# Kernel optimization log

Measured on AMD Instinct MI355X. Metric: run time of the kernel, lower is better.

Reference implementation:

```python
import jax, jax.numpy as jnp
import numpy as np

H, HID = 2, 64
N_USER, N_POST, N_ENT = 50000, 100000, 20000
EDGES = [("publish", 100000, N_USER, N_POST), ("repost", 200000, N_USER, N_POST), ("contain", 200000, N_POST, N_ENT), ("interact", 400000, N_USER, N_USER), ("follow", 400000, N_USER, N_USER), ("similar", 250000, N_POST, N_POST)]


def setup_inputs() -> dict:
    key = jax.random.key(0)
    ks = iter(jax.random.split(key, 64))
    d = {}
    d["x_post"] = jax.random.normal(next(ks), (N_POST, 768), jnp.float32)
    d["x_user"] = jax.random.normal(next(ks), (N_USER, 32), jnp.float32)
    d["x_entity"] = jax.random.normal(next(ks), (N_ENT, 64), jnp.float32)
    for name, E, ns, nd in EDGES:
        d["src_" + name] = jax.random.randint(next(ks), (E,), 0, ns, jnp.int32)
        d["dst_" + name] = jax.random.randint(next(ks), (E,), 0, nd, jnp.int32)
    def lin(k, o, i):
        return jax.random.normal(k, (o, i), jnp.float32) / np.sqrt(i)
    d["post_proj_w"] = lin(next(ks), HID, 768); d["post_proj_b"] = jnp.zeros((HID,), jnp.float32)
    d["user_proj_w"] = lin(next(ks), HID, 32); d["user_proj_b"] = jnp.zeros((HID,), jnp.float32)
    d["ent_proj_w"] = lin(next(ks), HID, 64); d["ent_proj_b"] = jnp.zeros((HID,), jnp.float32)
    # 2 layers x 6 relations of bipartite GATConv params, stacked
    d["W_src"] = jax.random.normal(next(ks), (2, 6, H * HID, HID), jnp.float32) / np.sqrt(HID)
    d["W_dst"] = jax.random.normal(next(ks), (2, 6, H * HID, HID), jnp.float32) / np.sqrt(HID)
    d["a_src"] = jax.random.normal(next(ks), (2, 6, H, HID), jnp.float32) * 0.1
    d["a_dst"] = jax.random.normal(next(ks), (2, 6, H, HID), jnp.float32) * 0.1
    d["gat_b"] = jnp.zeros((2, 6, HID), jnp.float32)
    d["cls_w1"] = lin(next(ks), HID // 2, HID); d["cls_b1"] = jnp.zeros((HID // 2,), jnp.float32)
    d["cls_w2"] = lin(next(ks), 1, HID // 2); d["cls_b2"] = jnp.zeros((1,), jnp.float32)
    return d


def _gat(x_src, x_dst, src, dst, w_s, w_d, a_s, a_d, b):
    """PyG GATConv, bipartite, heads=H, concat=False, no self loops."""
    n_dst = x_dst.shape[0]
    hs = (x_src @ w_s.T).reshape(-1, H, HID)   # [N_src, H, C]
    hd = (x_dst @ w_d.T).reshape(-1, H, HID)   # [N_dst, H, C]
    al_s = jnp.einsum("nhc,hc->nh", hs, a_s)
    al_d = jnp.einsum("nhc,hc->nh", hd, a_d)
    e = jax.nn.leaky_relu(al_s[src] + al_d[dst], negative_slope=0.2)  # [E, H]
    m = jax.ops.segment_max(e, dst, num_segments=n_dst)
    m = jnp.where(jnp.isfinite(m), m, 0.0)  # empty segments -> -inf, unused
    p = jnp.exp(e - m[dst])
    s = jax.ops.segment_sum(p, dst, num_segments=n_dst)
    alpha = p / (s[dst] + 1e-16)
    out = jax.ops.segment_sum(hs[src] * alpha[:, :, None], dst, num_segments=n_dst)
    return out.mean(axis=1) + b  # concat=False -> mean over heads, plus bias


def reference(x_post, x_user, x_entity, src_publish, dst_publish, src_repost, dst_repost, src_contain, dst_contain, src_interact, dst_interact, src_follow, dst_follow, src_similar, dst_similar, post_proj_w, post_proj_b, user_proj_w, user_proj_b, ent_proj_w, ent_proj_b, W_src, W_dst, a_src, a_dst, gat_b, cls_w1, cls_b1, cls_w2, cls_b2):
    h_post = x_post @ post_proj_w.T + post_proj_b
    h_user = x_user @ user_proj_w.T + user_proj_b
    h_ent = x_entity @ ent_proj_w.T + ent_proj_b
    for l in range(2):
        def g(r, xs, xd, s, dd):
            return _gat(xs, xd, s, dd, W_src[l, r], W_dst[l, r], a_src[l, r], a_dst[l, r], gat_b[l, r])
        new_post = (g(0, h_user, h_post, src_publish, dst_publish)
                    + g(1, h_user, h_post, src_repost, dst_repost)
                    + g(5, h_post, h_post, src_similar, dst_similar))
        new_ent = g(2, h_post, h_ent, src_contain, dst_contain)
        new_user = (g(3, h_user, h_user, src_interact, dst_interact)
                    + g(4, h_user, h_user, src_follow, dst_follow))
        h_post, h_user, h_ent = jax.nn.relu(new_post), jax.nn.relu(new_user), jax.nn.relu(new_ent)
    h = jax.nn.relu(h_post @ cls_w1.T + cls_b1)  # dropout is eval-mode identity
    return (h @ cls_w2.T + cls_b2).squeeze(-1)
```

## Files before the change

kernel.cpp:

```cpp
#include <hip/hip_runtime.h>

#define NPOST 100000
#define NUSER 50000
#define NENT  20000
#define NDTOT 420000
#define EACT  1350000
#define NSCANBLK 206
#define NT_AL 150000

typedef short short8 __attribute__((ext_vector_type(8)));
typedef float f32x4 __attribute__((ext_vector_type(4)));
typedef unsigned short ushort4v __attribute__((ext_vector_type(4)));

static __device__ __forceinline__ unsigned short f2bf(float x){
  union { float f; unsigned u; } v; v.f = x;
  unsigned r = v.u + 0x7FFF + ((v.u >> 16) & 1);
  return (unsigned short)(r >> 16);
}
static __device__ __forceinline__ float bf2f(unsigned short h){
  union { unsigned u; float f; } v; v.u = ((unsigned)h) << 16;
  return v.f;
}

struct EdgeMeta {
  const int* src[6];
  const int* dst[6];
  int E[6];
  int degoff[6];
};

struct PrepArgs {
  const float *Wp, *Wu, *We, *Wsrc, *Wdst, *asrc, *adst, *gatb;
  unsigned short *WpH, *WpL, *WuH, *WuL, *WeH, *WeL, *lbH, *lbL;
  float *weff_s, *weff_d, *bsum;
};

__global__ void k_prep(PrepArgs P){
  int idx = blockIdx.x * blockDim.x + threadIdx.x;
  if (idx < 49152){
    float x = P.Wp[idx];
    unsigned short h = f2bf(x);
    P.WpH[idx] = h; P.WpL[idx] = f2bf(x - bf2f(h));
  } else if (idx < 51200){
    int i = idx - 49152;
    float x = P.Wu[i];
    unsigned short h = f2bf(x);
    P.WuH[i] = h; P.WuL[i] = f2bf(x - bf2f(h));
  } else if (idx < 55296){
    int i = idx - 51200;
    float x = P.We[i];
    unsigned short h = f2bf(x);
    P.WeH[i] = h; P.WeL[i] = f2bf(x - bf2f(h));
  } else if (idx < 153600){
    int i = idx - 55296;
    const int off[6]  = {0, 24576, 40960, 49152, 73728, 90112};
    const int Ks[6]   = {384, 256, 128, 384, 256, 128};
    int seg = 5;
    #pragma unroll
    for (int s = 4; s >= 0; s--) if (i < off[s + 1]) seg = s;
    int l = seg / 3, type = seg % 3;
    int K = Ks[seg];
    int rem = i - off[seg];
    int n = rem / K, k = rem - n * K;
    int slot = k >> 7, head = (k >> 6) & 1, kk = k & 63;
    int rel;
    if (type == 0)      rel = (slot == 0) ? 0 : (slot == 1 ? 1 : 5);
    else if (type == 1) rel = (slot == 0) ? 3 : 4;
    else                rel = 2;
    int m = l * 6 + rel;
    float x = P.Wsrc[(size_t)m * 8192 + (head * 64 + n) * 64 + kk];
    unsigned short h = f2bf(x);
    P.lbH[i] = h; P.lbL[i] = f2bf(x - bf2f(h));
  } else if (idx < 156672){
    int i = idx - 153600;
    const float* W; const float* a; float* o; int j;
    if (i < 1536){ W = P.Wsrc; a = P.asrc; o = P.weff_s; j = i; }
    else         { W = P.Wdst; a = P.adst; o = P.weff_d; j = i - 1536; }
    int m = j >> 7;
    int rem = j & 127;
    int hh = rem >> 6, k = rem & 63;
    const float* Wm = W + (size_t)m * 8192;
    const float* am = a + (size_t)m * 128;
    float acc = 0.f;
    #pragma unroll 8
    for (int c = 0; c < 64; c++)
      acc += Wm[(hh * 64 + c) * 64 + k] * am[hh * 64 + c];
    o[j] = acc;
  } else if (idx < 157056){
    int i = idx - 156672;
    int c = i & 63;
    int lt = i >> 6;
    int l = lt / 3, t = lt % 3;
    float v;
    if (t == 0)      v = P.gatb[(l*6+0)*64+c] + P.gatb[(l*6+1)*64+c] + P.gatb[(l*6+5)*64+c];
    else if (t == 1) v = P.gatb[(l*6+3)*64+c] + P.gatb[(l*6+4)*64+c];
    else             v = P.gatb[(l*6+2)*64+c];
    P.bsum[lt * 64 + c] = v;
  }
}


__global__ void k_hist(EdgeMeta em, int* __restrict__ deg){
  const int map[5] = {0, 1, 3, 4, 5};
  int r = map[blockIdx.y];
  int e = blockIdx.x * blockDim.x + threadIdx.x;
  if (e >= em.E[r]) return;
  atomicAdd(&deg[em.degoff[r] + em.dst[r][e]], 1);
}

__global__ __launch_bounds__(256) void k_scanA(const int* __restrict__ deg,
                                               int* __restrict__ rowstart,
                                               int* __restrict__ blocksum){
  __shared__ int sums[256];
  int t = threadIdx.x;
  int base = blockIdx.x * 2048 + t * 8;
  int v[8]; int s = 0;
  #pragma unroll
  for (int i = 0; i < 8; i++){
    int j = base + i;
    v[i] = (j < NDTOT) ? deg[j] : 0;
    s += v[i];
  }
  sums[t] = s;
  __syncthreads();
  for (int off = 1; off < 256; off <<= 1){
    int x = (t >= off) ? sums[t - off] : 0;
    __syncthreads();
    sums[t] += x;
    __syncthreads();
  }
  int excl = (t > 0) ? sums[t - 1] : 0;
  if (t == 255) blocksum[blockIdx.x] = sums[255];
  int run = excl;
  #pragma unroll
  for (int i = 0; i < 8; i++){
    int j = base + i;
    if (j < NDTOT) rowstart[j] = run;
    run += v[i];
  }
}

__global__ __launch_bounds__(256) void k_scanB(int* __restrict__ blocksum){
  __shared__ int s[256];
  int t = threadIdx.x;
  s[t] = (t < NSCANBLK) ? blocksum[t] : 0;
  __syncthreads();
  for (int off = 1; off < 256; off <<= 1){
    int x = (t >= off) ? s[t - off] : 0;
    __syncthreads();
    s[t] += x;
    __syncthreads();
  }
  int excl = (t > 0) ? s[t - 1] : 0;
  if (t < NSCANBLK) blocksum[t] = excl;
}

__global__ void k_scanC(int* __restrict__ rowstart, const int* __restrict__ blocksum,
                        int* __restrict__ cursor){
  int j = blockIdx.x * blockDim.x + threadIdx.x;
  if (j < NDTOT){
    int v = rowstart[j] + blocksum[j >> 11];
    rowstart[j] = v;
    cursor[j] = v;
  }
  if (j == 0) rowstart[NDTOT] = EACT;
}

__global__ void k_scatter(EdgeMeta em, int* __restrict__ cursor,
                          int* __restrict__ csr_src, int* __restrict__ csr_row){
  const int map[5] = {0, 1, 3, 4, 5};
  int r = map[blockIdx.y];
  int e = blockIdx.x * blockDim.x + threadIdx.x;
  if (e >= em.E[r]) return;
  int d = em.dst[r][e];
  int w = em.degoff[r] + d;
  int pos = atomicAdd(&cursor[w], 1);
  csr_src[pos] = em.src[r][e];
  csr_row[pos] = w;
}


struct AlArgs {
  const float *h0, *h1;
  const float *ws, *wd;
  float *als, *ald;
  int layer;
};

static __device__ __forceinline__ float2 dot2w(const float4* hr, const float* __restrict__ w){
  const float4* w0 = (const float4*)w;
  const float4* w1 = (const float4*)(w + 64);
  float a0 = 0.f, a1 = 0.f;
  #pragma unroll
  for (int q = 0; q < 16; q++){
    float4 v = hr[q];
    float4 x0 = w0[q], x1 = w1[q];
    a0 += v.x*x0.x + v.y*x0.y + v.z*x0.z + v.w*x0.w;
    a1 += v.x*x1.x + v.y*x1.y + v.z*x1.z + v.w*x1.w;
  }
  return make_float2(a0, a1);
}

__global__ __launch_bounds__(256) void k_al_all(AlArgs A){
  int i = blockIdx.x * blockDim.x + threadIdx.x;
  if (i >= NT_AL) return;
  float4 hr[16];
  if (i < NPOST){
    int n = i;
    const float4* hp = (const float4*)(A.h0 + (size_t)n * 64);
    #pragma unroll
    for (int q = 0; q < 16; q++) hr[q] = hp[q];
    *(float2*)(A.als + (size_t)(300000 + n) * 2) = dot2w(hr, A.ws + 5 * 128);
    *(float2*)(A.ald + (size_t)(0      + n) * 2) = dot2w(hr, A.wd + 0 * 128);
    *(float2*)(A.ald + (size_t)(100000 + n) * 2) = dot2w(hr, A.wd + 1 * 128);
    *(float2*)(A.ald + (size_t)(320000 + n) * 2) = dot2w(hr, A.wd + 5 * 128);
  } else {
    int n = i - NPOST;
    const float4* hp = (const float4*)(A.h1 + (size_t)n * 64);
    #pragma unroll
    for (int q = 0; q < 16; q++) hr[q] = hp[q];
    *(float2*)(A.als + (size_t)(0      + n) * 2) = dot2w(hr, A.ws + 0 * 128);
    *(float2*)(A.als + (size_t)(50000  + n) * 2) = dot2w(hr, A.ws + 1 * 128);
    if (A.layer == 0){
      *(float2*)(A.als + (size_t)(200000 + n) * 2) = dot2w(hr, A.ws + 3 * 128);
      *(float2*)(A.als + (size_t)(250000 + n) * 2) = dot2w(hr, A.ws + 4 * 128);
      *(float2*)(A.ald + (size_t)(220000 + n) * 2) = dot2w(hr, A.wd + 3 * 128);
      *(float2*)(A.ald + (size_t)(270000 + n) * 2) = dot2w(hr, A.wd + 4 * 128);
    }
  }
}


struct EdgepArgs {
  const int *csr_src, *csr_row;
  const float *als, *ald;
  float2 *pcsr;
  int thr, off, nE;
};

__global__ __launch_bounds__(256) void k_edgep(EdgepArgs A){
  int e0 = blockIdx.x * blockDim.x + threadIdx.x;
  if (e0 >= A.nE) return;
  int e = e0 < A.thr ? e0 : e0 + A.off;
  int w = A.csr_row[e];
  int soffr;
  if      (w < 100000) soffr = 0;
  else if (w < 200000) soffr = 50000;
  else if (w < 270000) soffr = 200000;
  else if (w < 320000) soffr = 250000;
  else                 soffr = 300000;
  int sidx = A.csr_src[e];
  float2 as = *(const float2*)(A.als + (size_t)(soffr + sidx) * 2);
  float2 ad = *(const float2*)(A.ald + (size_t)w * 2);
  float e0v = as.x + ad.x, e1v = as.y + ad.y;
  e0v = e0v > 0.f ? e0v : 0.2f * e0v;
  e1v = e1v > 0.f ? e1v : 0.2f * e1v;
  A.pcsr[e] = make_float2(__expf(e0v), __expf(e1v));
}


static __device__ __forceinline__ int aswz(int row, int k){
  return row * 128 + ((((k >> 3) ^ (row & 7))) << 3) + (k & 7);
}

static __device__ __forceinline__ void agg_row(const int* __restrict__ csr_src,
                                               const float2* __restrict__ pcsr,
                                               const float* __restrict__ h, int l16,
                                               int rs, int re,
                                               f32x4& a0, f32x4& a1, float& s0, float& s1){
  int e = rs;
  for (; e + 3 < re; e += 4){
    int sa = csr_src[e];
    int sb = csr_src[e + 1];
    int sc = csr_src[e + 2];
    int sd = csr_src[e + 3];
    float2 pa = pcsr[e];
    float2 pb = pcsr[e + 1];
    float2 pc = pcsr[e + 2];
    float2 pd = pcsr[e + 3];
    f32x4 ha = *(const f32x4*)(h + (size_t)sa * 64 + l16 * 4);
    f32x4 hb = *(const f32x4*)(h + (size_t)sb * 64 + l16 * 4);
    f32x4 hc = *(const f32x4*)(h + (size_t)sc * 64 + l16 * 4);
    f32x4 hd = *(const f32x4*)(h + (size_t)sd * 64 + l16 * 4);
    #pragma unroll
    for (int j = 0; j < 4; j++){ a0[j] = fmaf(pa.x, ha[j], a0[j]); a1[j] = fmaf(pa.y, ha[j], a1[j]); }
    s0 += pa.x; s1 += pa.y;
    #pragma unroll
    for (int j = 0; j < 4; j++){ a0[j] = fmaf(pb.x, hb[j], a0[j]); a1[j] = fmaf(pb.y, hb[j], a1[j]); }
    s0 += pb.x; s1 += pb.y;
    #pragma unroll
    for (int j = 0; j < 4; j++){ a0[j] = fmaf(pc.x, hc[j], a0[j]); a1[j] = fmaf(pc.y, hc[j], a1[j]); }
    s0 += pc.x; s1 += pc.y;
    #pragma unroll
    for (int j = 0; j < 4; j++){ a0[j] = fmaf(pd.x, hd[j], a0[j]); a1[j] = fmaf(pd.y, hd[j], a1[j]); }
    s0 += pd.x; s1 += pd.y;
  }
  for (; e + 1 < re; e += 2){
    int sa = csr_src[e];
    int sb = csr_src[e + 1];
    float2 pa = pcsr[e];
    float2 pb = pcsr[e + 1];
    f32x4 ha = *(const f32x4*)(h + (size_t)sa * 64 + l16 * 4);
    f32x4 hb = *(const f32x4*)(h + (size_t)sb * 64 + l16 * 4);
    #pragma unroll
    for (int j = 0; j < 4; j++){ a0[j] = fmaf(pa.x, ha[j], a0[j]); a1[j] = fmaf(pa.y, ha[j], a1[j]); }
    s0 += pa.x; s1 += pa.y;
    #pragma unroll
    for (int j = 0; j < 4; j++){ a0[j] = fmaf(pb.x, hb[j], a0[j]); a1[j] = fmaf(pb.y, hb[j], a1[j]); }
    s0 += pb.x; s1 += pb.y;
  }
  if (e < re){
    int sa = csr_src[e];
    float2 pa = pcsr[e];
    f32x4 ha = *(const f32x4*)(h + (size_t)sa * 64 + l16 * 4);
    #pragma unroll
    for (int j = 0; j < 4; j++){ a0[j] = fmaf(pa.x, ha[j], a0[j]); a1[j] = fmaf(pa.y, ha[j], a1[j]); }
    s0 += pa.x; s1 += pa.y;
  }
}

struct FJob {
  const unsigned short *BH, *BL;
  const float *bias;
  float *C;
  int N, nslots, K;
  int wb0, wb1, wb2;
  int ss0, ss1, ss2;
};
struct FArgs {
  const int *rowstart, *csr_src;
  const float2 *pcsr;
  const float *h0, *h1;
  FJob j0, j1;
  int nb0;
};

__global__ __launch_bounds__(256) void k_fused(FArgs A){
  __shared__ __align__(16) unsigned short sAh[64 * 128];
  __shared__ __align__(16) unsigned short sAl[64 * 128];
  int b = blockIdx.x;
  FJob J = (b < A.nb0) ? A.j0 : A.j1;
  int boff = (b < A.nb0) ? 0 : A.nb0;
  int r0 = (b - boff) * 64;
  int t = threadIdx.x;
  int w = t >> 6, lane = t & 63;
  int q = lane >> 4, m15 = lane & 15;
  int g2 = t >> 4, l16 = t & 15;
  int wr = w & 1, wc = w >> 1;
  f32x4 acc[2][2];
  #pragma unroll
  for (int i = 0; i < 2; i++)
    #pragma unroll
    for (int j = 0; j < 2; j++)
      acc[i][j] = (f32x4){0.f, 0.f, 0.f, 0.f};

  for (int s = 0; s < J.nslots; s++){
    int wbase = (s == 0) ? J.wb0 : ((s == 1) ? J.wb1 : J.wb2);
    int ssel  = (s == 0) ? J.ss0 : ((s == 1) ? J.ss1 : J.ss2);
    const float* h = ssel ? A.h1 : A.h0;
    for (int rr = g2; rr < 64; rr += 16){
      int grow = r0 + rr;
      int rs = 0, re = 0;
      if (grow < J.N){
        int wg = wbase + grow;
        rs = A.rowstart[wg];
        re = A.rowstart[wg + 1];
      }
      f32x4 a0 = (f32x4){0.f,0.f,0.f,0.f};
      f32x4 a1 = (f32x4){0.f,0.f,0.f,0.f};
      float s0 = 0.f, s1 = 0.f;
      agg_row(A.csr_src, A.pcsr, h, l16, rs, re, a0, a1, s0, s1);
      float r0v = s0 > 0.f ? 0.5f / s0 : 0.f;
      float r1v = s1 > 0.f ? 0.5f / s1 : 0.f;
      ushort4v H0, H1, L0, L1;
      #pragma unroll
      for (int j = 0; j < 4; j++){
        float v0 = a0[j] * r0v;
        float v1 = a1[j] * r1v;
        unsigned short h0v = f2bf(v0); H0[j] = h0v; L0[j] = f2bf(v0 - bf2f(h0v));
        unsigned short h1v = f2bf(v1); H1[j] = h1v; L1[j] = f2bf(v1 - bf2f(h1v));
      }
      *(ushort4v*)(sAh + aswz(rr, l16 * 4))      = H0;
      *(ushort4v*)(sAh + aswz(rr, 64 + l16 * 4)) = H1;
      *(ushort4v*)(sAl + aswz(rr, l16 * 4))      = L0;
      *(ushort4v*)(sAl + aswz(rr, 64 + l16 * 4)) = L1;
    }
    __syncthreads();
    #pragma unroll
    for (int kc = 0; kc < 4; kc++){
      int gk = s * 128 + kc * 32;
      short8 ah[2], al_[2];
      #pragma unroll
      for (int i = 0; i < 2; i++){
        int mrow = wr * 32 + i * 16 + m15;
        ah[i]  = *(const short8*)(sAh + aswz(mrow, kc * 32 + q * 8));
        al_[i] = *(const short8*)(sAl + aswz(mrow, kc * 32 + q * 8));
      }
      #pragma unroll
      for (int j = 0; j < 2; j++){
        int bn = wc * 32 + j * 16 + m15;
        short8 bh = *(const short8*)(J.BH + (size_t)bn * J.K + gk + q * 8);
        short8 bl = *(const short8*)(J.BL + (size_t)bn * J.K + gk + q * 8);
        #pragma unroll
        for (int i = 0; i < 2; i++){
          acc[i][j] = __builtin_amdgcn_mfma_f32_16x16x32_bf16(ah[i],  bh, acc[i][j], 0, 0, 0);
          acc[i][j] = __builtin_amdgcn_mfma_f32_16x16x32_bf16(ah[i],  bl, acc[i][j], 0, 0, 0);
          acc[i][j] = __builtin_amdgcn_mfma_f32_16x16x32_bf16(al_[i], bh, acc[i][j], 0, 0, 0);
        }
      }
    }
    __syncthreads();
  }
  #pragma unroll
  for (int j = 0; j < 2; j++){
    int col = wc * 32 + j * 16 + m15;
    float bv = J.bias[col];
    #pragma unroll
    for (int i = 0; i < 2; i++){
      #pragma unroll
      for (int r = 0; r < 4; r++){
        int row = r0 + wr * 32 + i * 16 + q * 4 + r;
        if (row < J.N){
          float vv = acc[i][j][r] + bv;
          J.C[(size_t)row * 64 + col] = vv > 0.f ? vv : 0.f;
        }
      }
    }
  }
}


static __device__ __forceinline__ int swz(int row, int k){
  return row * 32 + ((((k >> 3) ^ ((row >> 2) & 3))) << 3) + (k & 7);
}

struct GemmJob {
  const float* A32;
  const unsigned short* AH; const unsigned short* AL;
  const unsigned short* BH; const unsigned short* BL;
  const float* bias; float* C;
  int N; int K;
};
struct GemmJobs { GemmJob j0, j1, j2; int nb0, nb1; };

template<int ASRC, int RELU>
__global__ __launch_bounds__(256) void k_mfgemm3(GemmJobs G){
  __shared__ __align__(16) unsigned short sAh[128 * 32];
  __shared__ __align__(16) unsigned short sAl[128 * 32];
  __shared__ __align__(16) unsigned short sBh[64 * 32];
  __shared__ __align__(16) unsigned short sBl[64 * 32];
  int b = blockIdx.x;
  GemmJob jb = G.j0;
  int boff = 0;
  if (b >= G.nb1){ jb = G.j2; boff = G.nb1; }
  else if (b >= G.nb0){ jb = G.j1; boff = G.nb0; }
  const float* A32 = jb.A32;
  const unsigned short* AH = jb.AH;
  const unsigned short* AL = jb.AL;
  const unsigned short* BH = jb.BH;
  const unsigned short* BL = jb.BL;
  int N = jb.N, K = jb.K;

  int t = threadIdx.x;
  int w = t >> 6, lane = t & 63;
  int q = lane >> 4, m15 = lane & 15;
  int r0 = (b - boff) * 128;
  f32x4 acc[2][4];
  #pragma unroll
  for (int i = 0; i < 2; i++)
    #pragma unroll
    for (int j = 0; j < 4; j++)
      acc[i][j] = (f32x4){0.f, 0.f, 0.f, 0.f};

  int arow = t >> 1, akb = (t & 1) * 16;
  int brow = t >> 2, bkb = (t & 3) * 8;

  for (int k0 = 0; k0 < K; k0 += 32){
    int gr = r0 + arow;
    if (ASRC == 0){
      float v[16];
      if (gr < N){
        const float4* ap = (const float4*)(A32 + (size_t)gr * K + k0 + akb);
        #pragma unroll
        for (int i = 0; i < 4; i++){
          float4 f = ap[i];
          v[i*4+0] = f.x; v[i*4+1] = f.y; v[i*4+2] = f.z; v[i*4+3] = f.w;
        }
      } else {
        #pragma unroll
        for (int i = 0; i < 16; i++) v[i] = 0.f;
      }
      short8 h0, h1, l0, l1;
      #pragma unroll
      for (int i = 0; i < 8; i++){
        unsigned short hh = f2bf(v[i]);
        h0[i] = (short)hh; l0[i] = (short)f2bf(v[i] - bf2f(hh));
        unsigned short hj = f2bf(v[8+i]);
        h1[i] = (short)hj; l1[i] = (short)f2bf(v[8+i] - bf2f(hj));
      }
      *(short8*)(sAh + swz(arow, akb))     = h0;
      *(short8*)(sAh + swz(arow, akb + 8)) = h1;
      *(short8*)(sAl + swz(arow, akb))     = l0;
      *(short8*)(sAl + swz(arow, akb + 8)) = l1;
    } else {
      short8 h0 = {0,0,0,0,0,0,0,0}, h1 = {0,0,0,0,0,0,0,0};
      short8 l0 = {0,0,0,0,0,0,0,0}, l1 = {0,0,0,0,0,0,0,0};
      if (gr < N){
        const short8* hp = (const short8*)(AH + (size_t)gr * K + k0 + akb);
        const short8* lp = (const short8*)(AL + (size_t)gr * K + k0 + akb);
        h0 = hp[0]; h1 = hp[1];
        l0 = lp[0]; l1 = lp[1];
      }
      *(short8*)(sAh + swz(arow, akb))     = h0;
      *(short8*)(sAh + swz(arow, akb + 8)) = h1;
      *(short8*)(sAl + swz(arow, akb))     = l0;
      *(short8*)(sAl + swz(arow, akb + 8)) = l1;
    }
    {
      short8 bh = *(const short8*)(BH + (size_t)brow * K + k0 + bkb);
      short8 bl = *(const short8*)(BL + (size_t)brow * K + k0 + bkb);
      *(short8*)(sBh + swz(brow, bkb)) = bh;
      *(short8*)(sBl + swz(brow, bkb)) = bl;
    }
    __syncthreads();
    short8 ah[2], al_[2];
    #pragma unroll
    for (int i = 0; i < 2; i++){
      int mrow = w * 32 + i * 16 + m15;
      ah[i]  = *(const short8*)(sAh + swz(mrow, q * 8));
      al_[i] = *(const short8*)(sAl + swz(mrow, q * 8));
    }
    #pragma unroll
    for (int j = 0; j < 4; j++){
      int bn = j * 16 + m15;
      short8 bh = *(const short8*)(sBh + swz(bn, q * 8));
      short8 bl = *(const short8*)(sBl + swz(bn, q * 8));
      #pragma unroll
      for (int i = 0; i < 2; i++){
        acc[i][j] = __builtin_amdgcn_mfma_f32_16x16x32_bf16(ah[i],  bh, acc[i][j], 0, 0, 0);
        acc[i][j] = __builtin_amdgcn_mfma_f32_16x16x32_bf16(ah[i],  bl, acc[i][j], 0, 0, 0);
        acc[i][j] = __builtin_amdgcn_mfma_f32_16x16x32_bf16(al_[i], bh, acc[i][j], 0, 0, 0);
      }
    }
    __syncthreads();
  }
  const float* bias = jb.bias;
  float* C = jb.C;
  #pragma unroll
  for (int j = 0; j < 4; j++){
    int col = j * 16 + m15;
    float bv = bias[col];
    #pragma unroll
    for (int i = 0; i < 2; i++){
      #pragma unroll
      for (int r = 0; r < 4; r++){
        int row = r0 + w * 32 + i * 16 + q * 4 + r;
        if (row < N){
          float vv = acc[i][j][r] + bv;
          if (RELU) vv = vv > 0.f ? vv : 0.f;
          C[(size_t)row * 64 + col] = vv;
        }
      }
    }
  }
}


__global__ __launch_bounds__(256) void k_classifier(const float* __restrict__ hpost,
                                                    const float* __restrict__ w1,
                                                    const float* __restrict__ b1,
                                                    const float* __restrict__ w2,
                                                    const float* __restrict__ b2,
                                                    float* __restrict__ out, int N){
  __shared__ float w1s[32 * 64];
  __shared__ float b1s[32];
  __shared__ float w2s[32];
  for (int i = threadIdx.x; i < 2048; i += 256) w1s[i] = w1[i];
  if (threadIdx.x < 32){
    b1s[threadIdx.x] = b1[threadIdx.x];
    w2s[threadIdx.x] = w2[threadIdx.x];
  }
  __syncthreads();
  float bias2 = b2[0];
  for (int n = blockIdx.x * blockDim.x + threadIdx.x; n < N; n += gridDim.x * blockDim.x){
    float4 hr[16];
    const float4* hp = (const float4*)(hpost + (size_t)n * 64);
    #pragma unroll
    for (int q = 0; q < 16; q++) hr[q] = hp[q];
    float o = bias2;
    #pragma unroll 4
    for (int j = 0; j < 32; j++){
      float dacc = b1s[j];
      const float4* wr = (const float4*)(w1s + j * 64);
      #pragma unroll
      for (int q = 0; q < 16; q++){
        float4 w = wr[q]; float4 v = hr[q];
        dacc += w.x*v.x + w.y*v.y + w.z*v.z + w.w*v.w;
      }
      dacc = dacc > 0.f ? dacc : 0.f;
      o += w2s[j] * dacc;
    }
    out[n] = o;
  }
}


static inline size_t align256(size_t x){ return (x + 255) & ~(size_t)255; }

extern "C" void kernel_launch(void* const* d_in, const int* in_sizes, int n_in,
                              void* d_out, int out_size, void* d_ws, size_t ws_size,
                              hipStream_t stream){
  (void)in_sizes; (void)n_in; (void)out_size; (void)ws_size;
  const float* x_post = (const float*)d_in[0];
  const float* x_user = (const float*)d_in[1];
  EdgeMeta em;
  for (int r = 0; r < 6; r++){
    em.src[r] = (const int*)d_in[3 + 2*r];
    em.dst[r] = (const int*)d_in[4 + 2*r];
  }
  const int Earr[6] = {100000, 200000, 200000, 400000, 400000, 250000};
  const int dgo[6]  = {0, 100000, 200000, 220000, 270000, 320000};
  for (int r = 0; r < 6; r++){ em.E[r] = Earr[r]; em.degoff[r] = dgo[r]; }

  const float* Wp   = (const float*)d_in[15]; const float* bp = (const float*)d_in[16];
  const float* Wu   = (const float*)d_in[17]; const float* bu = (const float*)d_in[18];
  const float* We   = (const float*)d_in[19];
  const float* Wsrc = (const float*)d_in[21];
  const float* Wdst = (const float*)d_in[22];
  const float* asrc = (const float*)d_in[23];
  const float* adst = (const float*)d_in[24];
  const float* gatb = (const float*)d_in[25];
  const float* cw1  = (const float*)d_in[26]; const float* cb1 = (const float*)d_in[27];
  const float* cw2  = (const float*)d_in[28]; const float* cb2 = (const float*)d_in[29];
  float* out = (float*)d_out;

  const int NN[2] = {NPOST, NUSER};

  char* p = (char*)d_ws;
  auto alloc = [&](size_t bytes){ char* r = p; p += align256(bytes); return r; };
  float* hA[2]; float* hB[2];
  for (int i = 0; i < 2; i++) hA[i] = (float*)alloc((size_t)NN[i] * 64 * 4);
  for (int i = 0; i < 2; i++) hB[i] = (float*)alloc((size_t)NN[i] * 64 * 4);
  float* als = (float*)alloc((size_t)400000 * 2 * 4);
  float* ald = (float*)alloc((size_t)NDTOT * 2 * 4);
  float* weff_s = (float*)alloc(1536 * 4);
  float* weff_d = (float*)alloc(1536 * 4);
  unsigned short* WpH = (unsigned short*)alloc(768 * 64 * 2);
  unsigned short* WpL = (unsigned short*)alloc(768 * 64 * 2);
  unsigned short* WuH = (unsigned short*)alloc(32 * 64 * 2);
  unsigned short* WuL = (unsigned short*)alloc(32 * 64 * 2);
  unsigned short* WeH = (unsigned short*)alloc(64 * 64 * 2);
  unsigned short* WeL = (unsigned short*)alloc(64 * 64 * 2);
  unsigned short* lbH = (unsigned short*)alloc(98304 * 2);
  unsigned short* lbL = (unsigned short*)alloc(98304 * 2);
  float* bsum   = (float*)alloc(6 * 64 * 4);
  int* deg      = (int*)alloc((size_t)NDTOT * 4);
  int* rowstart = (int*)alloc((size_t)(NDTOT + 1) * 4);
  int* cursor   = (int*)alloc((size_t)NDTOT * 4);
  int* csr_src  = (int*)alloc((size_t)EACT * 4);
  int* csr_row  = (int*)alloc((size_t)EACT * 4);
  float2* pcsr  = (float2*)alloc((size_t)EACT * 8);
  int* blocksum = (int*)alloc((size_t)NSCANBLK * 4);

  hipMemsetAsync(deg, 0, (size_t)NDTOT * 4, stream);
  k_hist<<<dim3(1563, 5), 256, 0, stream>>>(em, deg);
  k_scanA<<<NSCANBLK, 256, 0, stream>>>(deg, rowstart, blocksum);
  k_scanB<<<1, 256, 0, stream>>>(blocksum);
  k_scanC<<<(NDTOT + 255) / 256, 256, 0, stream>>>(rowstart, blocksum, cursor);
  k_scatter<<<dim3(1563, 5), 256, 0, stream>>>(em, cursor, csr_src, csr_row);

  PrepArgs P = {Wp, Wu, We, Wsrc, Wdst, asrc, adst, gatb,
                WpH, WpL, WuH, WuL, WeH, WeL, lbH, lbL,
                weff_s, weff_d, bsum};
  k_prep<<<614, 256, 0, stream>>>(P);

  GemmJobs GP;
  GP.j0 = {x_post, nullptr, nullptr, WpH, WpL, bp, hA[0], NPOST, 768};
  GP.j1 = {x_user, nullptr, nullptr, WuH, WuL, bu, hA[1], NUSER, 32};
  GP.j2 = GP.j1;
  GP.nb0 = 782; GP.nb1 = 1173;
  k_mfgemm3<0, 0><<<1173, 256, 0, stream>>>(GP);

  const int segoff[6] = {0, 24576, 40960, 49152, 73728, 90112};

  float* cur[2] = {hA[0], hA[1]};
  float* nxt[2] = {hB[0], hB[1]};

  for (int l = 0; l < 2; l++){
    AlArgs AA = {cur[0], cur[1], weff_s + l * 768, weff_d + l * 768, als, ald, l};
    k_al_all<<<(NT_AL + 255) / 256, 256, 0, stream>>>(AA);

    int nE  = (l == 0) ? EACT : 550000;
    int thr = (l == 0) ? EACT : 300000;
    int off = (l == 0) ? 0 : 800000;
    EdgepArgs EP = {csr_src, csr_row, als, ald, pcsr, thr, off, nE};
    k_edgep<<<(nE + 255) / 256, 256, 0, stream>>>(EP);

    FArgs FA;
    FA.rowstart = rowstart; FA.csr_src = csr_src; FA.pcsr = pcsr;
    FA.h0 = cur[0]; FA.h1 = cur[1];
    FA.j0 = {lbH + segoff[l*3+0], lbL + segoff[l*3+0], bsum + (l*3+0) * 64, nxt[0],
             NPOST, 3, 384, 0, 100000, 320000, 1, 1, 0};
    int grid;
    if (l == 0){
      FA.j1 = {lbH + segoff[l*3+1], lbL + segoff[l*3+1], bsum + (l*3+1) * 64, nxt[1],
               NUSER, 2, 256, 220000, 270000, 0, 1, 1, 0};
      FA.nb0 = 1563; grid = 1563 + 782;
    } else {
      FA.j1 = FA.j0;
      FA.nb0 = 1563; grid = 1563;
    }
    k_fused<<<grid, 256, 0, stream>>>(FA);

    for (int i = 0; i < 2; i++){ float* tmp = cur[i]; cur[i] = nxt[i]; nxt[i] = tmp; }
  }

  k_classifier<<<(NPOST + 255) / 256, 256, 0, stream>>>(cur[0], cw1, cb1, cw2, cb2, out, NPOST);
}
```

Before: 583.0 us.

## Fuse edge-softmax logits into aggregation and classifier into last fused layer

```diff
diff --git a/kernel.cpp b/kernel.cpp
--- a/kernel.cpp
+++ b/kernel.cpp
@@ -166,8 +166,7 @@
   if (j == 0) rowstart[NDTOT] = EACT;
 }
 
-__global__ void k_scatter(EdgeMeta em, int* __restrict__ cursor,
-                          int* __restrict__ csr_src, int* __restrict__ csr_row){
+__global__ void k_scatter(EdgeMeta em, int* __restrict__ cursor, int* __restrict__ csr_src){
   const int map[5] = {0, 1, 3, 4, 5};
   int r = map[blockIdx.y];
   int e = blockIdx.x * blockDim.x + threadIdx.x;
@@ -176,7 +175,6 @@
   int w = em.degoff[r] + d;
   int pos = atomicAdd(&cursor[w], 1);
   csr_src[pos] = em.src[r][e];
-  csr_row[pos] = w;
 }
 
 
@@ -231,91 +229,71 @@
 }
 
 
-struct EdgepArgs {
-  const int *csr_src, *csr_row;
-  const float *als, *ald;
-  float2 *pcsr;
-  int thr, off, nE;
-};
-
-__global__ __launch_bounds__(256) void k_edgep(EdgepArgs A){
-  int e0 = blockIdx.x * blockDim.x + threadIdx.x;
-  if (e0 >= A.nE) return;
-  int e = e0 < A.thr ? e0 : e0 + A.off;
-  int w = A.csr_row[e];
-  int soffr;
-  if      (w < 100000) soffr = 0;
-  else if (w < 200000) soffr = 50000;
-  else if (w < 270000) soffr = 200000;
-  else if (w < 320000) soffr = 250000;
-  else                 soffr = 300000;
-  int sidx = A.csr_src[e];
-  float2 as = *(const float2*)(A.als + (size_t)(soffr + sidx) * 2);
-  float2 ad = *(const float2*)(A.ald + (size_t)w * 2);
-  float e0v = as.x + ad.x, e1v = as.y + ad.y;
-  e0v = e0v > 0.f ? e0v : 0.2f * e0v;
-  e1v = e1v > 0.f ? e1v : 0.2f * e1v;
-  A.pcsr[e] = make_float2(__expf(e0v), __expf(e1v));
-}
-
-
 static __device__ __forceinline__ int aswz(int row, int k){
   return row * 128 + ((((k >> 3) ^ (row & 7))) << 3) + (k & 7);
 }
 
+static __device__ __forceinline__ void edge_p(const int* __restrict__ csr_src,
+                                              const float* __restrict__ als, float2 ad,
+                                              int e, int& s_out, float& px, float& py){
+  int sidx = csr_src[e];
+  float2 as = *(const float2*)(als + (size_t)sidx * 2);
+  float e0 = as.x + ad.x, e1 = as.y + ad.y;
+  e0 = e0 > 0.f ? e0 : 0.2f * e0;
+  e1 = e1 > 0.f ? e1 : 0.2f * e1;
+  px = __expf(e0); py = __expf(e1);
+  s_out = sidx;
+}
+
 static __device__ __forceinline__ void agg_row(const int* __restrict__ csr_src,
-                                               const float2* __restrict__ pcsr,
+                                               const float* __restrict__ als, float2 ad,
                                                const float* __restrict__ h, int l16,
                                                int rs, int re,
                                                f32x4& a0, f32x4& a1, float& s0, float& s1){
   int e = rs;
   for (; e + 3 < re; e += 4){
-    int sa = csr_src[e];
-    int sb = csr_src[e + 1];
-    int sc = csr_src[e + 2];
-    int sd = csr_src[e + 3];
-    float2 pa = pcsr[e];
-    float2 pb = pcsr[e + 1];
-    float2 pc = pcsr[e + 2];
-    float2 pd = pcsr[e + 3];
+    int sa, sb, sc, sd; float pax, pay, pbx, pby, pcx, pcy, pdx, pdy;
+    edge_p(csr_src, als, ad, e,     sa, pax, pay);
+    edge_p(csr_src, als, ad, e + 1, sb, pbx, pby);
+    edge_p(csr_src, als, ad, e + 2, sc, pcx, pcy);
+    edge_p(csr_src, als, ad, e + 3, sd, pdx, pdy);
     f32x4 ha = *(const f32x4*)(h + (size_t)sa * 64 + l16 * 4);
     f32x4 hb = *(const f32x4*)(h + (size_t)sb * 64 + l16 * 4);
     f32x4 hc = *(const f32x4*)(h + (size_t)sc * 64 + l16 * 4);
     f32x4 hd = *(const f32x4*)(h + (size_t)sd * 64 + l16 * 4);
     #pragma unroll
-    for (int j = 0; j < 4; j++){ a0[j] = fmaf(pa.x, ha[j], a0[j]); a1[j] = fmaf(pa.y, ha[j], a1[j]); }
-    s0 += pa.x; s1 += pa.y;
-    #pragma unroll
-    for (int j = 0; j < 4; j++){ a0[j] = fmaf(pb.x, hb[j], a0[j]); a1[j] = fmaf(pb.y, hb[j], a1[j]); }
-    s0 += pb.x; s1 += pb.y;
-    #pragma unroll
-    for (int j = 0; j < 4; j++){ a0[j] = fmaf(pc.x, hc[j], a0[j]); a1[j] = fmaf(pc.y, hc[j], a1[j]); }
-    s0 += pc.x; s1 += pc.y;
-    #pragma unroll
-    for (int j = 0; j < 4; j++){ a0[j] = fmaf(pd.x, hd[j], a0[j]); a1[j] = fmaf(pd.y, hd[j], a1[j]); }
-    s0 += pd.x; s1 += pd.y;
+    for (int j = 0; j < 4; j++){ a0[j] = fmaf(pax, ha[j], a0[j]); a1[j] = fmaf(pay, ha[j], a1[j]); }
+    s0 += pax; s1 += pay;
+    #pragma unroll
+    for (int j = 0; j < 4; j++){ a0[j] = fmaf(pbx, hb[j], a0[j]); a1[j] = fmaf(pby, hb[j], a1[j]); }
+    s0 += pbx; s1 += pby;
+    #pragma unroll
+    for (int j = 0; j < 4; j++){ a0[j] = fmaf(pcx, hc[j], a0[j]); a1[j] = fmaf(pcy, hc[j], a1[j]); }
+    s0 += pcx; s1 += pcy;
+    #pragma unroll
+    for (int j = 0; j < 4; j++){ a0[j] = fmaf(pdx, hd[j], a0[j]); a1[j] = fmaf(pdy, hd[j], a1[j]); }
+    s0 += pdx; s1 += pdy;
   }
   for (; e + 1 < re; e += 2){
-    int sa = csr_src[e];
-    int sb = csr_src[e + 1];
-    float2 pa = pcsr[e];
-    float2 pb = pcsr[e + 1];
+    int sa, sb; float pax, pay, pbx, pby;
+    edge_p(csr_src, als, ad, e,     sa, pax, pay);
+    edge_p(csr_src, als, ad, e + 1, sb, pbx, pby);
     f32x4 ha = *(const f32x4*)(h + (size_t)sa * 64 + l16 * 4);
     f32x4 hb = *(const f32x4*)(h + (size_t)sb * 64 + l16 * 4);
     #pragma unroll
-    for (int j = 0; j < 4; j++){ a0[j] = fmaf(pa.x, ha[j], a0[j]); a1[j] = fmaf(pa.y, ha[j], a1[j]); }
-    s0 += pa.x; s1 += pa.y;
-    #pragma unroll
-    for (int j = 0; j < 4; j++){ a0[j] = fmaf(pb.x, hb[j], a0[j]); a1[j] = fmaf(pb.y, hb[j], a1[j]); }
-    s0 += pb.x; s1 += pb.y;
+    for (int j = 0; j < 4; j++){ a0[j] = fmaf(pax, ha[j], a0[j]); a1[j] = fmaf(pay, ha[j], a1[j]); }
+    s0 += pax; s1 += pay;
+    #pragma unroll
+    for (int j = 0; j < 4; j++){ a0[j] = fmaf(pbx, hb[j], a0[j]); a1[j] = fmaf(pby, hb[j], a1[j]); }
+    s0 += pbx; s1 += pby;
   }
   if (e < re){
-    int sa = csr_src[e];
-    float2 pa = pcsr[e];
+    int sa; float pax, pay;
+    edge_p(csr_src, als, ad, e, sa, pax, pay);
     f32x4 ha = *(const f32x4*)(h + (size_t)sa * 64 + l16 * 4);
     #pragma unroll
-    for (int j = 0; j < 4; j++){ a0[j] = fmaf(pa.x, ha[j], a0[j]); a1[j] = fmaf(pa.y, ha[j], a1[j]); }
-    s0 += pa.x; s1 += pa.y;
+    for (int j = 0; j < 4; j++){ a0[j] = fmaf(pax, ha[j], a0[j]); a1[j] = fmaf(pay, ha[j], a1[j]); }
+    s0 += pax; s1 += pay;
   }
 }
 
@@ -326,18 +304,23 @@
   int N, nslots, K;
   int wb0, wb1, wb2;
   int ss0, ss1, ss2;
+  int as0, as1, as2;
 };
 struct FArgs {
   const int *rowstart, *csr_src;
-  const float2 *pcsr;
+  const float *als, *ald;
   const float *h0, *h1;
   FJob j0, j1;
   int nb0;
+  const float *cw1, *cb1, *cw2, *cb2;
+  float *out;
 };
 
+template<int CLS>
 __global__ __launch_bounds__(256) void k_fused(FArgs A){
-  __shared__ __align__(16) unsigned short sAh[64 * 128];
-  __shared__ __align__(16) unsigned short sAl[64 * 128];
+  __shared__ __align__(16) unsigned short sbuf[2 * 64 * 128];
+  unsigned short* sAh = sbuf;
+  unsigned short* sAl = sbuf + 64 * 128;
   int b = blockIdx.x;
   FJob J = (b < A.nb0) ? A.j0 : A.j1;
   int boff = (b < A.nb0) ? 0 : A.nb0;
@@ -357,19 +340,23 @@
   for (int s = 0; s < J.nslots; s++){
     int wbase = (s == 0) ? J.wb0 : ((s == 1) ? J.wb1 : J.wb2);
     int ssel  = (s == 0) ? J.ss0 : ((s == 1) ? J.ss1 : J.ss2);
+    int aoff  = (s == 0) ? J.as0 : ((s == 1) ? J.as1 : J.as2);
     const float* h = ssel ? A.h1 : A.h0;
+    const float* als = A.als + (size_t)aoff * 2;
     for (int rr = g2; rr < 64; rr += 16){
       int grow = r0 + rr;
       int rs = 0, re = 0;
+      float2 ad = make_float2(0.f, 0.f);
       if (grow < J.N){
         int wg = wbase + grow;
         rs = A.rowstart[wg];
         re = A.rowstart[wg + 1];
+        ad = *(const float2*)(A.ald + (size_t)wg * 2);
       }
       f32x4 a0 = (f32x4){0.f,0.f,0.f,0.f};
       f32x4 a1 = (f32x4){0.f,0.f,0.f,0.f};
       float s0 = 0.f, s1 = 0.f;
-      agg_row(A.csr_src, A.pcsr, h, l16, rs, re, a0, a1, s0, s1);
+      agg_row(A.csr_src, als, ad, h, l16, rs, re, a0, a1, s0, s1);
       float r0v = s0 > 0.f ? 0.5f / s0 : 0.f;
       float r1v = s1 > 0.f ? 0.5f / s1 : 0.f;
       ushort4v H0, H1, L0, L1;
@@ -411,19 +398,66 @@
     }
     __syncthreads();
   }
-  #pragma unroll
-  for (int j = 0; j < 2; j++){
-    int col = wc * 32 + j * 16 + m15;
-    float bv = J.bias[col];
-    #pragma unroll
-    for (int i = 0; i < 2; i++){
+  if (!CLS){
+    #pragma unroll
+    for (int j = 0; j < 2; j++){
+      int col = wc * 32 + j * 16 + m15;
+      float bv = J.bias[col];
       #pragma unroll
-      for (int r = 0; r < 4; r++){
-        int row = r0 + wr * 32 + i * 16 + q * 4 + r;
-        if (row < J.N){
+      for (int i = 0; i < 2; i++){
+        #pragma unroll
+        for (int r = 0; r < 4; r++){
+          int row = r0 + wr * 32 + i * 16 + q * 4 + r;
+          if (row < J.N){
+            float vv = acc[i][j][r] + bv;
+            J.C[(size_t)row * 64 + col] = vv > 0.f ? vv : 0.f;
+          }
+        }
+      }
+    }
+  } else {
+    float* ht  = (float*)sbuf;
+    float* w1s = ht + 64 * 68;
+    float* b1s = w1s + 2048;
+    float* w2s = b1s + 32;
+    #pragma unroll
+    for (int j = 0; j < 2; j++){
+      int col = wc * 32 + j * 16 + m15;
+      float bv = J.bias[col];
+      #pragma unroll
+      for (int i = 0; i < 2; i++){
+        #pragma unroll
+        for (int r = 0; r < 4; r++){
+          int lrow = wr * 32 + i * 16 + q * 4 + r;
           float vv = acc[i][j][r] + bv;
-          J.C[(size_t)row * 64 + col] = vv > 0.f ? vv : 0.f;
+          ht[lrow * 68 + col] = vv > 0.f ? vv : 0.f;
         }
+      }
+    }
+    for (int i = t; i < 2048; i += 256) w1s[i] = A.cw1[i];
+    if (t < 32){ b1s[t] = A.cb1[t]; w2s[t] = A.cw2[t]; }
+    __syncthreads();
+    if (t < 64){
+      int row = r0 + t;
+      if (row < J.N){
+        float4 hr[16];
+        const float4* hp = (const float4*)(ht + t * 68);
+        #pragma unroll
+        for (int q16 = 0; q16 < 16; q16++) hr[q16] = hp[q16];
+        float o = A.cb2[0];
+        #pragma unroll 4
+        for (int j = 0; j < 32; j++){
+          float dacc = b1s[j];
+          const float4* wr_ = (const float4*)(w1s + j * 64);
+          #pragma unroll
+          for (int q16 = 0; q16 < 16; q16++){
+            float4 wv = wr_[q16]; float4 v = hr[q16];
+            dacc += wv.x*v.x + wv.y*v.y + wv.z*v.z + wv.w*v.w;
+          }
+          dacc = dacc > 0.f ? dacc : 0.f;
+          o += w2s[j] * dacc;
+        }
+        A.out[row] = o;
       }
     }
   }
@@ -562,45 +596,6 @@
         }
       }
     }
-  }
-}
-
-
-__global__ __launch_bounds__(256) void k_classifier(const float* __restrict__ hpost,
-                                                    const float* __restrict__ w1,
-                                                    const float* __restrict__ b1,
-                                                    const float* __restrict__ w2,
-                                                    const float* __restrict__ b2,
-                                                    float* __restrict__ out, int N){
-  __shared__ float w1s[32 * 64];
-  __shared__ float b1s[32];
-  __shared__ float w2s[32];
-  for (int i = threadIdx.x; i < 2048; i += 256) w1s[i] = w1[i];
-  if (threadIdx.x < 32){
-    b1s[threadIdx.x] = b1[threadIdx.x];
-    w2s[threadIdx.x] = w2[threadIdx.x];
-  }
-  __syncthreads();
-  float bias2 = b2[0];
-  for (int n = blockIdx.x * blockDim.x + threadIdx.x; n < N; n += gridDim.x * blockDim.x){
-    float4 hr[16];
-    const float4* hp = (const float4*)(hpost + (size_t)n * 64);
-    #pragma unroll
-    for (int q = 0; q < 16; q++) hr[q] = hp[q];
-    float o = bias2;
-    #pragma unroll 4
-    for (int j = 0; j < 32; j++){
-      float dacc = b1s[j];
-      const float4* wr = (const float4*)(w1s + j * 64);
-      #pragma unroll
-      for (int q = 0; q < 16; q++){
-        float4 w = wr[q]; float4 v = hr[q];
-        dacc += w.x*v.x + w.y*v.y + w.z*v.z + w.w*v.w;
-      }
-      dacc = dacc > 0.f ? dacc : 0.f;
-      o += w2s[j] * dacc;
-    }
-    out[n] = o;
   }
 }
 
@@ -658,8 +653,6 @@
   int* rowstart = (int*)alloc((size_t)(NDTOT + 1) * 4);
   int* cursor   = (int*)alloc((size_t)NDTOT * 4);
   int* csr_src  = (int*)alloc((size_t)EACT * 4);
-  int* csr_row  = (int*)alloc((size_t)EACT * 4);
-  float2* pcsr  = (float2*)alloc((size_t)EACT * 8);
   int* blocksum = (int*)alloc((size_t)NSCANBLK * 4);
 
   hipMemsetAsync(deg, 0, (size_t)NDTOT * 4, stream);
@@ -667,7 +660,7 @@
   k_scanA<<<NSCANBLK, 256, 0, stream>>>(deg, rowstart, blocksum);
   k_scanB<<<1, 256, 0, stream>>>(blocksum);
   k_scanC<<<(NDTOT + 255) / 256, 256, 0, stream>>>(rowstart, blocksum, cursor);
-  k_scatter<<<dim3(1563, 5), 256, 0, stream>>>(em, cursor, csr_src, csr_row);
+  k_scatter<<<dim3(1563, 5), 256, 0, stream>>>(em, cursor, csr_src);
 
   PrepArgs P = {Wp, Wu, We, Wsrc, Wdst, asrc, adst, gatb,
                 WpH, WpL, WuH, WuL, WeH, WeL, lbH, lbL,
@@ -690,30 +683,23 @@
     AlArgs AA = {cur[0], cur[1], weff_s + l * 768, weff_d + l * 768, als, ald, l};
     k_al_all<<<(NT_AL + 255) / 256, 256, 0, stream>>>(AA);
 
-    int nE  = (l == 0) ? EACT : 550000;
-    int thr = (l == 0) ? EACT : 300000;
-    int off = (l == 0) ? 0 : 800000;
-    EdgepArgs EP = {csr_src, csr_row, als, ald, pcsr, thr, off, nE};
-    k_edgep<<<(nE + 255) / 256, 256, 0, stream>>>(EP);
-
     FArgs FA;
-    FA.rowstart = rowstart; FA.csr_src = csr_src; FA.pcsr = pcsr;
+    FA.rowstart = rowstart; FA.csr_src = csr_src;
+    FA.als = als; FA.ald = ald;
     FA.h0 = cur[0]; FA.h1 = cur[1];
+    FA.cw1 = cw1; FA.cb1 = cb1; FA.cw2 = cw2; FA.cb2 = cb2; FA.out = out;
     FA.j0 = {lbH + segoff[l*3+0], lbL + segoff[l*3+0], bsum + (l*3+0) * 64, nxt[0],
-             NPOST, 3, 384, 0, 100000, 320000, 1, 1, 0};
-    int grid;
+             NPOST, 3, 384, 0, 100000, 320000, 1, 1, 0, 0, 50000, 300000};
     if (l == 0){
       FA.j1 = {lbH + segoff[l*3+1], lbL + segoff[l*3+1], bsum + (l*3+1) * 64, nxt[1],
-               NUSER, 2, 256, 220000, 270000, 0, 1, 1, 0};
-      FA.nb0 = 1563; grid = 1563 + 782;
+               NUSER, 2, 256, 220000, 270000, 0, 1, 1, 0, 200000, 250000, 0};
+      FA.nb0 = 1563;
+      k_fused<0><<<1563 + 782, 256, 0, stream>>>(FA);
     } else {
       FA.j1 = FA.j0;
-      FA.nb0 = 1563; grid = 1563;
-    }
-    k_fused<<<grid, 256, 0, stream>>>(FA);
-
+      FA.nb0 = 1563;
+      k_fused<1><<<1563, 256, 0, stream>>>(FA);
+    }
     for (int i = 0; i < 2; i++){ float* tmp = cur[i]; cur[i] = nxt[i]; nxt[i] = tmp; }
   }
-
-  k_classifier<<<(NPOST + 255) / 256, 256, 0, stream>>>(cur[0], cw1, cb1, cw2, cb2, out, NPOST);
-}
+}
```

Result: no change. 593.4 us (+1.8%).
